# Performance work log

Measured on AMD Instinct MI355X. Metric: run time of the kernel, lower is better.

Reference implementation:

```python
import jax, jax.numpy as jnp
import numpy as np
import math

DIM = 512
HEADS = 8
DIM_HEAD = DIM // HEADS
TIME_DIM = 512
EPS = 1e-5


def _ln(x, g, b):
    m = jnp.mean(x, axis=-1, keepdims=True)
    v = jnp.var(x, axis=-1, keepdims=True)
    return (x - m) * jax.lax.rsqrt(v + EPS) * g + b


def setup_inputs() -> dict:
    key = jax.random.key(0)
    ks = jax.random.split(key, 16)
    s = 0.02
    return {
        "con_features": jax.random.normal(ks[0], (4, 1024, DIM), jnp.float32),
        "diff_features": jax.random.normal(ks[1], (4, 1024, DIM), jnp.float32),
        "time_emb": jax.random.normal(ks[2], (4, TIME_DIM), jnp.float32),
        "ln_con_g": jnp.ones((DIM,), jnp.float32),
        "ln_con_b": jnp.zeros((DIM,), jnp.float32),
        "ln_diff_g": jnp.ones((DIM,), jnp.float32),
        "ln_diff_b": jnp.zeros((DIM,), jnp.float32),
        "wq": jax.random.normal(ks[3], (DIM, DIM), jnp.float32) * s,
        "wk": jax.random.normal(ks[4], (DIM, DIM), jnp.float32) * s,
        "wv": jax.random.normal(ks[5], (DIM, DIM), jnp.float32) * s,
        "w_out": jax.random.normal(ks[6], (DIM, DIM), jnp.float32) * s,
        "b_out": jnp.zeros((DIM,), jnp.float32),
        "w_emd1": jax.random.normal(ks[7], (TIME_DIM, 2 * DIM), jnp.float32) * s,
        "b_emd1": jnp.zeros((2 * DIM,), jnp.float32),
        "w_emd2": jax.random.normal(ks[8], (2 * DIM, 2 * DIM), jnp.float32) * s,
        "b_emd2": jnp.zeros((2 * DIM,), jnp.float32),
        "mlp_ln_g": jnp.ones((DIM,), jnp.float32),
        "mlp_ln_b": jnp.zeros((DIM,), jnp.float32),
        "mlp_w1": jax.random.normal(ks[9], (DIM, DIM), jnp.float32) * s,
        "mlp_b1": jnp.zeros((DIM,), jnp.float32),
        "mlp_w2": jax.random.normal(ks[10], (DIM, DIM), jnp.float32) * s,
        "mlp_b2": jnp.zeros((DIM,), jnp.float32),
    }


def reference(con_features, diff_features, time_emb,
              ln_con_g, ln_con_b, ln_diff_g, ln_diff_b,
              wq, wk, wv, w_out, b_out,
              w_emd1, b_emd1, w_emd2, b_emd2,
              mlp_ln_g, mlp_ln_b, mlp_w1, mlp_b1, mlp_w2, mlp_b2):
    b, n, _ = diff_features.shape
    fea_q = _ln(diff_features, ln_diff_g, ln_diff_b)
    fea_kv = _ln(con_features, ln_con_g, ln_con_b)
    # projections (no bias) + split heads: b n (h d) -> b h n d
    def heads(x):
        return x.reshape(b, n, HEADS, DIM_HEAD).transpose(0, 2, 1, 3)
    q = heads(fea_q @ wq)
    k = heads(fea_kv @ wk)
    v = heads(fea_kv @ wv)
    # 2D FFT over (n, d), ortho norm
    qf = jnp.fft.fft2(q, axes=(-2, -1), norm="ortho")
    kf = jnp.fft.fft2(k, axes=(-2, -1), norm="ortho")
    dots = jnp.einsum("bhnd,bhmd->bhnm", qf, jnp.conj(kf))  # q @ k^H
    attn_c = jnp.fft.ifft2(dots, axes=(-2, -1), norm="ortho")
    mag = jnp.sqrt(attn_c.real ** 2 + attn_c.imag ** 2)
    attn = jax.nn.softmax(mag, axis=-1) / math.sqrt(DIM_HEAD)
    out = jnp.einsum("bhnm,bhmd->bhnd", attn, v)
    out = out.transpose(0, 2, 1, 3).reshape(b, n, DIM)  # b h n d -> b n (h d)
    # global per-sample normalization over (n, dim); torch.std uses ddof=1
    mu = jnp.mean(out, axis=(-2, -1), keepdims=True)
    sd = jnp.std(out, axis=(-2, -1), keepdims=True, ddof=1)
    out1 = (out - mu) / sd
    # FiLM from time embedding
    t = jax.nn.silu(time_emb @ w_emd1 + b_emd1)
    t = t @ w_emd2 + b_emd2
    mean_t, std_t = jnp.split(t, 2, axis=-1)
    out1 = out1 * std_t[:, None, :] + mean_t[:, None, :]
    out1 = out1 @ w_out + b_out
    # FeedForward: LN -> Linear -> GELU(exact) -> Linear
    h = _ln(out1, mlp_ln_g, mlp_ln_b)
    h = jax.nn.gelu(h @ mlp_w1 + mlp_b1, approximate=False)
    return h @ mlp_w2 + mlp_b2
```

## Files before the change

### kernel.cpp

```cpp
#include <hip/hip_runtime.h>
#include <math.h>


typedef _Float16 f16;
typedef _Float16 f16x4 __attribute__((ext_vector_type(4)));
typedef _Float16 f16x8 __attribute__((ext_vector_type(8)));
typedef float f32x4 __attribute__((ext_vector_type(4)));

#define ROWS 4096
#define NTOK 1024
#define NB   4
#define NH   8
#define DH   64

__device__ __forceinline__ void glds16(const f16* g, f16* l) {
    __builtin_amdgcn_global_load_lds((const __attribute__((address_space(1))) void*)g,
                                     (__attribute__((address_space(3))) void*)l, 16, 0, 0);
}

struct PrepArgs { const float* src[6]; f16* dst[6]; };

__device__ __forceinline__ void ln_row(const float* __restrict__ x, const float* __restrict__ g,
                                       const float* __restrict__ bb, f16* __restrict__ o, int lane) {
    float v[8]; float s = 0.f;
#pragma unroll
    for (int j = 0; j < 8; j++) { v[j] = x[lane + 64 * j]; s += v[j]; }
#pragma unroll
    for (int d = 32; d >= 1; d >>= 1) s += __shfl_xor(s, d, 64);
    float mean = s * (1.f / 512.f);
    float q = 0.f;
#pragma unroll
    for (int j = 0; j < 8; j++) { float t = v[j] - mean; q += t * t; }
#pragma unroll
    for (int d = 32; d >= 1; d >>= 1) q += __shfl_xor(q, d, 64);
    float inv = rsqrtf(q * (1.f / 512.f) + 1e-5f);
#pragma unroll
    for (int j = 0; j < 8; j++) {
        int c = lane + 64 * j;
        o[c] = (f16)((v[j] - mean) * inv * g[c] + bb[c]);
    }
}

__global__ __launch_bounds__(256) void k_pre(PrepArgs pa, float* stats,
                                             const float* __restrict__ b_emd1, const float* __restrict__ b_emd2,
                                             float* __restrict__ tbacc, float* __restrict__ filmp,
                                             const float* __restrict__ diff, const float* __restrict__ g_dif,
                                             const float* __restrict__ b_dif, f16* __restrict__ A16,
                                             const float* __restrict__ con, const float* __restrict__ g_con,
                                             const float* __restrict__ b_con, f16* __restrict__ C16) {
    __shared__ float smem[1056];
    const int id = blockIdx.x, tid = threadIdx.x;
    if (id < 16) {
        int o = id * 256 + tid;
        tbacc[o] = b_emd1[o & 1023];
        filmp[o] = b_emd2[o & 1023];
        if (id == 0 && tid < 8) stats[tid] = 0.f;
    } else if (id < 1552) {
        int pid = id - 16;
        int m = pid >> 8, rem = pid & 255;
        int o0 = (rem & 15) * 32, i0 = (rem >> 4) * 32;
        int tx = tid & 31, ty = tid >> 5;
        const float* src = pa.src[m];
        f16* dst = pa.dst[m];
        for (int r = ty; r < 32; r += 8)
            smem[r * 33 + tx] = src[(i0 + r) * 512 + o0 + tx];
        __syncthreads();
        for (int r = ty; r < 32; r += 8)
            dst[(o0 + r) * 512 + i0 + tx] = (f16)smem[tx * 33 + r];
    } else {
        int lane = tid & 63, wid = tid >> 6;
        long row = (long)(id - 1552) * 4 + wid;
        if (row < ROWS) ln_row(diff + row * 512, g_dif, b_dif, A16 + row * 512, lane);
        else { long r = row - ROWS; ln_row(con + r * 512, g_con, b_con, C16 + r * 512, lane); }
    }
}

__global__ __launch_bounds__(256) void k_qkv(const f16* __restrict__ A16, const f16* __restrict__ C16,
                                             const f16* __restrict__ wqT, const f16* __restrict__ wkT,
                                             const f16* __restrict__ wvT,
                                             f16* __restrict__ Qh, f16* __restrict__ Kf, f16* __restrict__ Vt,
                                             const float* __restrict__ temb, const float* __restrict__ w_emd1,
                                             float* __restrict__ tbacc) {
    __shared__ __attribute__((aligned(16))) f16 sh[128 * 128 + 64 * 128];
    const int id = blockIdx.x, tid = threadIdx.x;
    if (id >= 768) {
        float* tsh = (float*)sh;
        int pid = id - 768;
        int c = (pid & 3) * 256 + tid;
        int k0 = (pid >> 2) * 32;
        if (tid < 128) tsh[(tid >> 5) * 32 + (tid & 31)] = temb[(tid >> 5) * 512 + k0 + (tid & 31)];
        __syncthreads();
        float a0 = 0.f, a1 = 0.f, a2 = 0.f, a3 = 0.f;
#pragma unroll 8
        for (int k = 0; k < 32; k++) {
            float w = w_emd1[(k0 + k) * 1024 + c];
            a0 += tsh[k] * w; a1 += tsh[32 + k] * w; a2 += tsh[64 + k] * w; a3 += tsh[96 + k] * w;
        }
        atomicAdd(&tbacc[c], a0);        atomicAdd(&tbacc[1024 + c], a1);
        atomicAdd(&tbacc[2048 + c], a2); atomicAdd(&tbacc[3072 + c], a3);
        return;
    }
    f16* Ash = sh;
    f16* Bsh = sh + 128 * 128;
    const int z = id >> 8;
    const f16* A  = (z == 0) ? A16 : C16;
    const f16* BT = (z == 0) ? wqT : (z == 1) ? wkT : wvT;
    const int lane = tid & 63, wid = tid >> 6;
    const int quad = lane >> 4, l15 = lane & 15;
    const int m0 = (id & 31) * 128, n0 = ((id >> 5) & 7) * 64;
    const int wm = (wid >> 1) * 64, wn = (wid & 1) * 32;
    const int srow = lane >> 4, slot = lane & 15;
    f32x4 acc[4][2] = {};
    for (int kk = 0; kk < 512; kk += 128) {
        if (kk) __syncthreads();
#pragma unroll
        for (int c = 0; c < 8; c++) {
            int r = c * 16 + 4 * wid + srow;
            int j = slot ^ (r & 7);
            glds16(&A[(long)(m0 + r) * 512 + kk + 8 * j], &Ash[(c * 16 + 4 * wid) * 128]);
        }
#pragma unroll
        for (int c = 0; c < 4; c++) {
            int r = c * 16 + 4 * wid + srow;
            int j = slot ^ (r & 7);
            glds16(&BT[(long)(n0 + r) * 512 + kk + 8 * j], &Bsh[(c * 16 + 4 * wid) * 128]);
        }
        __syncthreads();
#pragma unroll
        for (int ks = 0; ks < 4; ks++) {
            const int rslot = ((ks * 4 + quad) ^ (l15 & 7)) * 8;
            f16x8 af[4], bf[2];
#pragma unroll
            for (int t = 0; t < 4; t++)
                af[t] = *(const f16x8*)&Ash[(wm + t * 16 + l15) * 128 + rslot];
#pragma unroll
            for (int t = 0; t < 2; t++)
                bf[t] = *(const f16x8*)&Bsh[(wn + t * 16 + l15) * 128 + rslot];
#pragma unroll
            for (int mt = 0; mt < 4; mt++)
#pragma unroll
                for (int nt = 0; nt < 2; nt++)
                    acc[mt][nt] = __builtin_amdgcn_mfma_f32_16x16x32_f16(af[mt], bf[nt], acc[mt][nt], 0, 0, 0);
        }
    }
    __syncthreads();
    const int bb = m0 >> 10, nn0 = m0 & 1023, h = (id >> 5) & 7;
    if (z <= 1) {
#pragma unroll
        for (int mt = 0; mt < 4; mt++)
#pragma unroll
            for (int nt = 0; nt < 2; nt++)
#pragma unroll
                for (int r = 0; r < 4; r++)
                    sh[(wm + mt * 16 + quad * 4 + r) * 72 + wn + nt * 16 + l15] = (f16)acc[mt][nt][r];
        __syncthreads();
        f16* dst = (z == 0) ? Qh : Kf;
        long basebh = ((long)(bb * NH + h)) * NTOK * DH;
#pragma unroll
        for (int q2 = 0; q2 < 4; q2++) {
            int c = tid + q2 * 256;
            int row = c >> 3, col = (c & 7) * 8;
            int n = nn0 + row;
            int nr = (z == 1) ? ((NTOK - n) & (NTOK - 1)) : n;
            *(f16x8*)&dst[basebh + (long)nr * DH + col] = *(const f16x8*)&sh[row * 72 + col];
        }
    } else {
#pragma unroll
        for (int mt = 0; mt < 4; mt++)
#pragma unroll
            for (int nt = 0; nt < 2; nt++)
#pragma unroll
                for (int r = 0; r < 4; r++)
                    sh[(wn + nt * 16 + l15) * 136 + wm + mt * 16 + quad * 4 + r] = (f16)acc[mt][nt][r];
        __syncthreads();
        long basev = ((long)(bb * NH + h)) * DH * NTOK;
#pragma unroll
        for (int q2 = 0; q2 < 4; q2++) {
            int c = tid + q2 * 256;
            int d = c >> 4, col = (c & 15) * 8;
            *(f16x8*)&Vt[basev + (long)d * NTOK + nn0 + col] = *(const f16x8*)&sh[d * 136 + col];
        }
    }
}

template <int EPI>
__global__ __launch_bounds__(256) void k_gemm64(const f16* __restrict__ A, const f16* __restrict__ BT,
                                                const float* __restrict__ bias, void* __restrict__ dstv) {
    __shared__ __attribute__((aligned(16))) f16 Ash[64 * 128];
    __shared__ __attribute__((aligned(16))) f16 Bsh[64 * 128];
    const int tid = threadIdx.x;
    const int lane = tid & 63, wid = tid >> 6;
    const int quad = lane >> 4, l15 = lane & 15;
    const int m0 = blockIdx.x * 64, n0 = blockIdx.y * 64;
    const int wm = (wid >> 1) * 32, wn = (wid & 1) * 32;
    const int srow = lane >> 4, slot = lane & 15;
    f32x4 acc[2][2] = {};
    for (int kk = 0; kk < 512; kk += 128) {
        if (kk) __syncthreads();
#pragma unroll
        for (int c = 0; c < 4; c++) {
            int r = c * 16 + 4 * wid + srow;
            int j = slot ^ (r & 7);
            glds16(&A[(long)(m0 + r) * 512 + kk + 8 * j], &Ash[(c * 16 + 4 * wid) * 128]);
            glds16(&BT[(long)(n0 + r) * 512 + kk + 8 * j], &Bsh[(c * 16 + 4 * wid) * 128]);
        }
        __syncthreads();
#pragma unroll
        for (int ks = 0; ks < 4; ks++) {
            const int rslot = ((ks * 4 + quad) ^ (l15 & 7)) * 8;
            f16x8 af[2], bf[2];
#pragma unroll
            for (int t = 0; t < 2; t++) {
                af[t] = *(const f16x8*)&Ash[(wm + t * 16 + l15) * 128 + rslot];
                bf[t] = *(const f16x8*)&Bsh[(wn + t * 16 + l15) * 128 + rslot];
            }
#pragma unroll
            for (int mt = 0; mt < 2; mt++)
#pragma unroll
                for (int nt = 0; nt < 2; nt++)
                    acc[mt][nt] = __builtin_amdgcn_mfma_f32_16x16x32_f16(af[mt], bf[nt], acc[mt][nt], 0, 0, 0);
        }
    }
#pragma unroll
    for (int mt = 0; mt < 2; mt++)
#pragma unroll
        for (int nt = 0; nt < 2; nt++)
#pragma unroll
            for (int r = 0; r < 4; r++) {
                int gm = m0 + wm + mt * 16 + quad * 4 + r;
                int gn = n0 + wn + nt * 16 + l15;
                float v = acc[mt][nt][r];
                if (EPI == 3) {
                    float x = v + bias[gn];
                    ((f16*)dstv)[(long)gm * 512 + gn] = (f16)(0.5f * x * (1.0f + erff(x * 0.70710678f)));
                } else {
                    ((float*)dstv)[(long)gm * 512 + gn] = v + bias[gn];
                }
            }
}

__global__ __launch_bounds__(256) void k_gemm2f(const f16* __restrict__ aout16, const float* __restrict__ stats,
                                                const float* __restrict__ filmp,
                                                const f16* __restrict__ BT, const float* __restrict__ bias,
                                                float* __restrict__ out1) {
    __shared__ __attribute__((aligned(16))) f16 Ash[64 * 128];
    __shared__ __attribute__((aligned(16))) f16 Bsh[64 * 128];
    __shared__ float scsh[512], shsh[512];
    const int tid = threadIdx.x;
    const int lane = tid & 63, wid = tid >> 6;
    const int quad = lane >> 4, l15 = lane & 15;
    const int m0 = blockIdx.x * 64, n0 = blockIdx.y * 64;
    const int wm = (wid >> 1) * 32, wn = (wid & 1) * 32;
    const int srow = lane >> 4, slot = lane & 15;
    const int b = m0 >> 10;
    {
        float sum = stats[b * 2], sq = stats[b * 2 + 1];
        const float M = 524288.f;
        float mu = sum / M;
        float isd = rsqrtf((sq - sum * mu) / (M - 1.f));
        for (int c = tid; c < 512; c += 256) {
            float sc = isd * filmp[b * 1024 + 512 + c];
            scsh[c] = sc;
            shsh[c] = filmp[b * 1024 + c] - mu * sc;
        }
    }
    __syncthreads();
    f32x4 acc[2][2] = {};
    for (int kk = 0; kk < 512; kk += 128) {
        if (kk) __syncthreads();
        const int j = slot ^ ((4 * wid + srow) & 7);
        const int gcol = kk + 8 * j;
        float sc[8], sf[8];
        *(float4*)&sc[0] = *(const float4*)&scsh[gcol];
        *(float4*)&sc[4] = *(const float4*)&scsh[gcol + 4];
        *(float4*)&sf[0] = *(const float4*)&shsh[gcol];
        *(float4*)&sf[4] = *(const float4*)&shsh[gcol + 4];
#pragma unroll
        for (int c = 0; c < 4; c++) {
            int r = c * 16 + 4 * wid + srow;
            f16x8 v = *(const f16x8*)&aout16[(long)(m0 + r) * 512 + gcol];
            f16x8 y;
#pragma unroll
            for (int e = 0; e < 8; e++) y[e] = (f16)((float)v[e] * sc[e] + sf[e]);
            *(f16x8*)&Ash[(c * 16 + 4 * wid) * 128 + lane * 8] = y;
            glds16(&BT[(long)(n0 + r) * 512 + kk + 8 * j], &Bsh[(c * 16 + 4 * wid) * 128]);
        }
        __syncthreads();
#pragma unroll
        for (int ks = 0; ks < 4; ks++) {
            const int rslot = ((ks * 4 + quad) ^ (l15 & 7)) * 8;
            f16x8 af[2], bf[2];
#pragma unroll
            for (int t = 0; t < 2; t++) {
                af[t] = *(const f16x8*)&Ash[(wm + t * 16 + l15) * 128 + rslot];
                bf[t] = *(const f16x8*)&Bsh[(wn + t * 16 + l15) * 128 + rslot];
            }
#pragma unroll
            for (int mt = 0; mt < 2; mt++)
#pragma unroll
                for (int nt = 0; nt < 2; nt++)
                    acc[mt][nt] = __builtin_amdgcn_mfma_f32_16x16x32_f16(af[mt], bf[nt], acc[mt][nt], 0, 0, 0);
        }
    }
#pragma unroll
    for (int mt = 0; mt < 2; mt++)
#pragma unroll
        for (int nt = 0; nt < 2; nt++)
#pragma unroll
            for (int r = 0; r < 4; r++) {
                int gm = m0 + wm + mt * 16 + quad * 4 + r;
                int gn = n0 + wn + nt * 16 + l15;
                out1[(long)gm * 512 + gn] = acc[mt][nt][r] + bias[gn];
            }
}

__global__ __launch_bounds__(256) void k_attn(const f16* __restrict__ Q, const f16* __restrict__ Kf,
                                              const f16* __restrict__ Vt, f16* __restrict__ out,
                                              float* __restrict__ stats,
                                              const float* __restrict__ tbacc, const float* __restrict__ w_emd2,
                                              float* __restrict__ filmp) {
    __shared__ __attribute__((aligned(16))) f16 Ksh[128 * 64];
    __shared__ __attribute__((aligned(16))) f16 Vsh[64 * 128];
    __shared__ __attribute__((aligned(16))) f16 PshT[4 * 16 * 136];
    __shared__ float rbuf[8];
    const int id = blockIdx.x, tid = threadIdx.x;
    if (id >= 512) {
        float* tsh = (float*)Ksh;
        int pid = id - 512;
        int c = (pid & 3) * 256 + tid;
        int k0 = (pid >> 2) * 32;
        if (tid < 128) {
            float v = tbacc[(tid >> 5) * 1024 + k0 + (tid & 31)];
            tsh[(tid >> 5) * 32 + (tid & 31)] = v / (1.f + __expf(-v));
        }
        __syncthreads();
        float a0 = 0.f, a1 = 0.f, a2 = 0.f, a3 = 0.f;
#pragma unroll 8
        for (int k = 0; k < 32; k++) {
            float w = w_emd2[(k0 + k) * 1024 + c];
            a0 += tsh[k] * w; a1 += tsh[32 + k] * w; a2 += tsh[64 + k] * w; a3 += tsh[96 + k] * w;
        }
        atomicAdd(&filmp[c], a0);        atomicAdd(&filmp[1024 + c], a1);
        atomicAdd(&filmp[2048 + c], a2); atomicAdd(&filmp[3072 + c], a3);
        return;
    }
    const int lane = tid & 63, wid = tid >> 6;
    const int quad = lane >> 4, l15 = lane & 15;
    const int bh = id & 31;
    const int b = bh >> 3, h = bh & 7, q0 = (id >> 5) * 64;
    const f16* Qbh = Q + (long)bh * NTOK * DH;
    const f16* Kbh = Kf + (long)bh * NTOK * DH;
    const f16* Vbh = Vt + (long)bh * DH * NTOK;
    const int rl = lane >> 3, jj8 = (lane & 7) ^ rl;
    const int rl4 = lane >> 4, jjv = (lane & 15) ^ (4 * wid + rl4);
    const int qrow = q0 + wid * 16 + l15;
    f16x8 qf[2];
    qf[0] = *(const f16x8*)&Qbh[(long)qrow * DH + quad * 8];
    qf[1] = *(const f16x8*)&Qbh[(long)qrow * DH + 32 + quad * 8];
    f32x4 O[4] = {};
    float l_acc = 0.f;
    f16* Pw = PshT + wid * 16 * 136;

    for (int k0 = 0; k0 < NTOK; k0 += 128) {
        if (k0) __syncthreads();
#pragma unroll
        for (int c = 0; c < 4; c++) {
            int rk = c * 32 + 8 * wid + rl;
            glds16(&Kbh[(long)(k0 + rk) * DH + 8 * jj8], &Ksh[(c * 32 + 8 * wid) * 64]);
        }
#pragma unroll
        for (int c = 0; c < 4; c++) {
            int rv = c * 16 + 4 * wid + rl4;
            glds16(&Vbh[(long)rv * NTOK + k0 + 8 * jjv], &Vsh[(c * 16 + 4 * wid) * 128]);
        }
        __syncthreads();
        f32x4 st[8] = {};
#pragma unroll
        for (int ks = 0; ks < 2; ks++) {
            const int slot = ((ks * 4 + quad) ^ (l15 & 7)) * 8;
#pragma unroll
            for (int nt = 0; nt < 8; nt++) {
                f16x8 kf = *(const f16x8*)&Ksh[(nt * 16 + l15) * 64 + slot];
                st[nt] = __builtin_amdgcn_mfma_f32_16x16x32_f16(kf, qf[ks], st[nt], 0, 0, 0);
            }
        }
#pragma unroll
        for (int nt = 0; nt < 8; nt++) {
            float p0 = __expf(fminf(fabsf(st[nt][0]) - 8.f, 11.f));
            float p1 = __expf(fminf(fabsf(st[nt][1]) - 8.f, 11.f));
            float p2 = __expf(fminf(fabsf(st[nt][2]) - 8.f, 11.f));
            float p3 = __expf(fminf(fabsf(st[nt][3]) - 8.f, 11.f));
            l_acc += (p0 + p1) + (p2 + p3);
            f16x4 pk = { (f16)p0, (f16)p1, (f16)p2, (f16)p3 };
            *(f16x4*)&Pw[l15 * 136 + 16 * nt + quad * 4] = pk;
        }
#pragma unroll
        for (int ks = 0; ks < 4; ks++) {
            f16x8 pf = *(const f16x8*)&Pw[l15 * 136 + 32 * ks + quad * 8];
            const int vslot = ((ks * 4 + quad) ^ l15) * 8;
#pragma unroll
            for (int vt = 0; vt < 4; vt++) {
                f16x8 vf = *(const f16x8*)&Vsh[(vt * 16 + l15) * 128 + vslot];
                O[vt] = __builtin_amdgcn_mfma_f32_16x16x32_f16(pf, vf, O[vt], 0, 0, 0);
            }
        }
    }
    l_acc += __shfl_xor(l_acc, 16, 64);
    l_acc += __shfl_xor(l_acc, 32, 64);
    float lb[4];
#pragma unroll
    for (int r = 0; r < 4; r++) lb[r] = 0.125f / __shfl(l_acc, quad * 4 + r, 64);
    float lsum = 0.f, lsq = 0.f;
#pragma unroll
    for (int t = 0; t < 4; t++)
#pragma unroll
        for (int r = 0; r < 4; r++) {
            float v = O[t][r] * lb[r];
            int gn = q0 + wid * 16 + quad * 4 + r;
            int gc = h * DH + t * 16 + l15;
            out[((long)b * NTOK + gn) * 512 + gc] = (f16)v;
            lsum += v; lsq += v * v;
        }
#pragma unroll
    for (int d = 32; d >= 1; d >>= 1) { lsum += __shfl_xor(lsum, d, 64); lsq += __shfl_xor(lsq, d, 64); }
    if (lane == 0) { rbuf[wid] = lsum; rbuf[4 + wid] = lsq; }
    __syncthreads();
    if (tid == 0) {
        atomicAdd(&stats[b * 2], rbuf[0] + rbuf[1] + rbuf[2] + rbuf[3]);
        atomicAdd(&stats[b * 2 + 1], rbuf[4] + rbuf[5] + rbuf[6] + rbuf[7]);
    }
}

__global__ __launch_bounds__(256) void k_ln2(const float* __restrict__ x, const float* __restrict__ g,
                                             const float* __restrict__ bb, f16* __restrict__ o) {
    int lane = threadIdx.x & 63, wid = threadIdx.x >> 6;
    long row = (long)blockIdx.x * 4 + wid;
    ln_row(x + row * 512, g, bb, o + row * 512, lane);
}

extern "C" void kernel_launch(void* const* d_in, const int* in_sizes, int n_in,
                              void* d_out, int out_size, void* d_ws, size_t ws_size,
                              hipStream_t stream) {
    const float* con      = (const float*)d_in[0];
    const float* diff     = (const float*)d_in[1];
    const float* temb     = (const float*)d_in[2];
    const float* ln_con_g = (const float*)d_in[3];
    const float* ln_con_b = (const float*)d_in[4];
    const float* ln_dif_g = (const float*)d_in[5];
    const float* ln_dif_b = (const float*)d_in[6];
    const float* wq       = (const float*)d_in[7];
    const float* wk       = (const float*)d_in[8];
    const float* wv       = (const float*)d_in[9];
    const float* w_out    = (const float*)d_in[10];
    const float* b_out    = (const float*)d_in[11];
    const float* w_emd1   = (const float*)d_in[12];
    const float* b_emd1   = (const float*)d_in[13];
    const float* w_emd2   = (const float*)d_in[14];
    const float* b_emd2   = (const float*)d_in[15];
    const float* mlp_ln_g = (const float*)d_in[16];
    const float* mlp_ln_b = (const float*)d_in[17];
    const float* mlp_w1   = (const float*)d_in[18];
    const float* mlp_b1   = (const float*)d_in[19];
    const float* mlp_w2   = (const float*)d_in[20];
    const float* mlp_b2   = (const float*)d_in[21];
    float* outp = (float*)d_out;

    char* ws = (char*)d_ws;
    size_t off = 0;
    auto alloc = [&](size_t bytes) { void* p = ws + off; off += (bytes + 255) & ~(size_t)255; return p; };
    f16*   A16   = (f16*)alloc((size_t)ROWS * 512 * 2);
    f16*   C16   = (f16*)alloc((size_t)ROWS * 512 * 2);
    f16*   Qh    = (f16*)alloc((size_t)ROWS * 512 * 2);
    f16*   Kf    = (f16*)alloc((size_t)ROWS * 512 * 2);
    f16*   Vt    = (f16*)alloc((size_t)ROWS * 512 * 2);
    f16*   aout16= (f16*)alloc((size_t)ROWS * 512 * 2);
    f16*   wqT   = (f16*)alloc(512 * 512 * 2);
    f16*   wkT   = (f16*)alloc(512 * 512 * 2);
    f16*   wvT   = (f16*)alloc(512 * 512 * 2);
    f16*   woT   = (f16*)alloc(512 * 512 * 2);
    f16*   w1T   = (f16*)alloc(512 * 512 * 2);
    f16*   w2T   = (f16*)alloc(512 * 512 * 2);
    float* tbacc = (float*)alloc(4 * 1024 * 4);
    float* filmp = (float*)alloc(4 * 1024 * 4);
    float* stats = (float*)alloc(256);
    float* out1  = (float*)Qh;
    f16*   X3    = A16;
    f16*   X4    = C16;

    PrepArgs pa;
    pa.src[0] = wq;  pa.src[1] = wk;  pa.src[2] = wv;
    pa.src[3] = w_out; pa.src[4] = mlp_w1; pa.src[5] = mlp_w2;
    pa.dst[0] = wqT; pa.dst[1] = wkT; pa.dst[2] = wvT;
    pa.dst[3] = woT; pa.dst[4] = w1T; pa.dst[5] = w2T;

    k_pre<<<dim3(3600), dim3(256), 0, stream>>>(pa, stats, b_emd1, b_emd2, tbacc, filmp,
                                                diff, ln_dif_g, ln_dif_b, A16,
                                                con, ln_con_g, ln_con_b, C16);
    k_qkv<<<dim3(832), dim3(256), 0, stream>>>(A16, C16, wqT, wkT, wvT, Qh, Kf, Vt,
                                               temb, w_emd1, tbacc);
    k_attn<<<dim3(640), dim3(256), 0, stream>>>(Qh, Kf, Vt, aout16, stats,
                                                tbacc, w_emd2, filmp);
    k_gemm2f<<<dim3(64, 8), dim3(256), 0, stream>>>(aout16, stats, filmp, woT, b_out, out1);
    k_ln2<<<dim3(1024), dim3(256), 0, stream>>>(out1, mlp_ln_g, mlp_ln_b, X3);
    k_gemm64<3><<<dim3(64, 8), dim3(256), 0, stream>>>(X3, w1T, mlp_b1, (void*)X4);
    k_gemm64<4><<<dim3(64, 8), dim3(256), 0, stream>>>(X4, w2T, mlp_b2, (void*)outp);
}
```

Baseline: 184.6 us.

## Fuse MLP LayerNorm into GEMMs via row stats and widen attention query tiles

The out-projection GEMM now writes fp16 output and accumulates per-row sum and sum-of-squares with atomics. The next GEMM applies the LayerNorm while staging A into shared memory, so the separate LN kernel and the fp32 round-trip go away. The attention kernel now handles 32 query rows per wave (128 per block), which halves the block count and reuses each K/V tile across twice as many queries. Risks: computing variance as E[x^2]-mu^2 from fp16-rounded values loses precision, the A-tile load is no longer async, and with fewer attention blocks occupancy drops.

```diff
diff --git a/kernel.cpp b/kernel.cpp
--- a/kernel.cpp
+++ b/kernel.cpp
@@ -44,6 +44,7 @@
 __global__ __launch_bounds__(256) void k_pre(PrepArgs pa, float* stats,
                                              const float* __restrict__ b_emd1, const float* __restrict__ b_emd2,
                                              float* __restrict__ tbacc, float* __restrict__ filmp,
+                                             float* __restrict__ rstats,
                                              const float* __restrict__ diff, const float* __restrict__ g_dif,
                                              const float* __restrict__ b_dif, f16* __restrict__ A16,
                                              const float* __restrict__ con, const float* __restrict__ g_con,
@@ -55,8 +56,10 @@
         tbacc[o] = b_emd1[o & 1023];
         filmp[o] = b_emd2[o & 1023];
         if (id == 0 && tid < 8) stats[tid] = 0.f;
-    } else if (id < 1552) {
-        int pid = id - 16;
+    } else if (id < 48) {
+        rstats[(id - 16) * 256 + tid] = 0.f;
+    } else if (id < 1584) {
+        int pid = id - 48;
         int m = pid >> 8, rem = pid & 255;
         int o0 = (rem & 15) * 32, i0 = (rem >> 4) * 32;
         int tx = tid & 31, ty = tid >> 5;
@@ -69,7 +72,7 @@
             dst[(o0 + r) * 512 + i0 + tx] = (f16)smem[tx * 33 + r];
     } else {
         int lane = tid & 63, wid = tid >> 6;
-        long row = (long)(id - 1552) * 4 + wid;
+        long row = (long)(id - 1584) * 4 + wid;
         if (row < ROWS) ln_row(diff + row * 512, g_dif, b_dif, A16 + row * 512, lane);
         else { long r = row - ROWS; ln_row(con + r * 512, g_con, b_con, C16 + r * 512, lane); }
     }
@@ -183,66 +186,146 @@
     }
 }
 
-template <int EPI>
-__global__ __launch_bounds__(256) void k_gemm64(const f16* __restrict__ A, const f16* __restrict__ BT,
-                                                const float* __restrict__ bias, void* __restrict__ dstv) {
-    __shared__ __attribute__((aligned(16))) f16 Ash[64 * 128];
-    __shared__ __attribute__((aligned(16))) f16 Bsh[64 * 128];
-    const int tid = threadIdx.x;
+__global__ __launch_bounds__(256) void k_attn(const f16* __restrict__ Q, const f16* __restrict__ Kf,
+                                              const f16* __restrict__ Vt, f16* __restrict__ out,
+                                              float* __restrict__ stats,
+                                              const float* __restrict__ tbacc, const float* __restrict__ w_emd2,
+                                              float* __restrict__ filmp) {
+    __shared__ __attribute__((aligned(16))) f16 Ksh[128 * 64];
+    __shared__ __attribute__((aligned(16))) f16 Vsh[64 * 128];
+    __shared__ __attribute__((aligned(16))) f16 PshT[4 * 32 * 136];
+    __shared__ float rbuf[8];
+    const int id = blockIdx.x, tid = threadIdx.x;
+    if (id >= 256) {
+        float* tsh = (float*)Ksh;
+        int pid = id - 256;
+        int c = (pid & 3) * 256 + tid;
+        int k0 = (pid >> 2) * 32;
+        if (tid < 128) {
+            float v = tbacc[(tid >> 5) * 1024 + k0 + (tid & 31)];
+            tsh[(tid >> 5) * 32 + (tid & 31)] = v / (1.f + __expf(-v));
+        }
+        __syncthreads();
+        float a0 = 0.f, a1 = 0.f, a2 = 0.f, a3 = 0.f;
+#pragma unroll 8
+        for (int k = 0; k < 32; k++) {
+            float w = w_emd2[(k0 + k) * 1024 + c];
+            a0 += tsh[k] * w; a1 += tsh[32 + k] * w; a2 += tsh[64 + k] * w; a3 += tsh[96 + k] * w;
+        }
+        atomicAdd(&filmp[c], a0);        atomicAdd(&filmp[1024 + c], a1);
+        atomicAdd(&filmp[2048 + c], a2); atomicAdd(&filmp[3072 + c], a3);
+        return;
+    }
     const int lane = tid & 63, wid = tid >> 6;
     const int quad = lane >> 4, l15 = lane & 15;
-    const int m0 = blockIdx.x * 64, n0 = blockIdx.y * 64;
-    const int wm = (wid >> 1) * 32, wn = (wid & 1) * 32;
-    const int srow = lane >> 4, slot = lane & 15;
-    f32x4 acc[2][2] = {};
-    for (int kk = 0; kk < 512; kk += 128) {
-        if (kk) __syncthreads();
+    const int bh = id & 31;
+    const int b = bh >> 3, hh = bh & 7, q0 = (id >> 5) * 128;
+    const f16* Qbh = Q + (long)bh * NTOK * DH;
+    const f16* Kbh = Kf + (long)bh * NTOK * DH;
+    const f16* Vbh = Vt + (long)bh * DH * NTOK;
+    const int rl = lane >> 3, jj8 = (lane & 7) ^ rl;
+    const int rl4 = lane >> 4, jjv = (lane & 15) ^ (4 * wid + rl4);
+    const int qbase = q0 + wid * 32;
+    f16x8 qf[2][2];
+#pragma unroll
+    for (int h = 0; h < 2; h++) {
+        qf[h][0] = *(const f16x8*)&Qbh[(long)(qbase + 16 * h + l15) * DH + quad * 8];
+        qf[h][1] = *(const f16x8*)&Qbh[(long)(qbase + 16 * h + l15) * DH + 32 + quad * 8];
+    }
+    f32x4 O0[4] = {}, O1[4] = {};
+    float l0 = 0.f, l1 = 0.f;
+    f16* Pw = PshT + wid * 32 * 136;
+
+    for (int k0 = 0; k0 < NTOK; k0 += 128) {
+        if (k0) __syncthreads();
 #pragma unroll
         for (int c = 0; c < 4; c++) {
-            int r = c * 16 + 4 * wid + srow;
-            int j = slot ^ (r & 7);
-            glds16(&A[(long)(m0 + r) * 512 + kk + 8 * j], &Ash[(c * 16 + 4 * wid) * 128]);
-            glds16(&BT[(long)(n0 + r) * 512 + kk + 8 * j], &Bsh[(c * 16 + 4 * wid) * 128]);
-        }
-        __syncthreads();
+            int rk = c * 32 + 8 * wid + rl;
+            glds16(&Kbh[(long)(k0 + rk) * DH + 8 * jj8], &Ksh[(c * 32 + 8 * wid) * 64]);
+        }
+#pragma unroll
+        for (int c = 0; c < 4; c++) {
+            int rv = c * 16 + 4 * wid + rl4;
+            glds16(&Vbh[(long)rv * NTOK + k0 + 8 * jjv], &Vsh[(c * 16 + 4 * wid) * 128]);
+        }
+        __syncthreads();
+        f32x4 st0[8] = {}, st1[8] = {};
+#pragma unroll
+        for (int ks = 0; ks < 2; ks++) {
+            const int slot = ((ks * 4 + quad) ^ (l15 & 7)) * 8;
+#pragma unroll
+            for (int nt = 0; nt < 8; nt++) {
+                f16x8 kf = *(const f16x8*)&Ksh[(nt * 16 + l15) * 64 + slot];
+                st0[nt] = __builtin_amdgcn_mfma_f32_16x16x32_f16(kf, qf[0][ks], st0[nt], 0, 0, 0);
+                st1[nt] = __builtin_amdgcn_mfma_f32_16x16x32_f16(kf, qf[1][ks], st1[nt], 0, 0, 0);
+            }
+        }
+#pragma unroll
+        for (int nt = 0; nt < 8; nt++) {
+            float p0 = __expf(fminf(fabsf(st0[nt][0]) - 8.f, 11.f));
+            float p1 = __expf(fminf(fabsf(st0[nt][1]) - 8.f, 11.f));
+            float p2 = __expf(fminf(fabsf(st0[nt][2]) - 8.f, 11.f));
+            float p3 = __expf(fminf(fabsf(st0[nt][3]) - 8.f, 11.f));
+            l0 += (p0 + p1) + (p2 + p3);
+            f16x4 pk0 = { (f16)p0, (f16)p1, (f16)p2, (f16)p3 };
+            *(f16x4*)&Pw[l15 * 136 + 16 * nt + quad * 4] = pk0;
+            float u0 = __expf(fminf(fabsf(st1[nt][0]) - 8.f, 11.f));
+            float u1 = __expf(fminf(fabsf(st1[nt][1]) - 8.f, 11.f));
+            float u2 = __expf(fminf(fabsf(st1[nt][2]) - 8.f, 11.f));
+            float u3 = __expf(fminf(fabsf(st1[nt][3]) - 8.f, 11.f));
+            l1 += (u0 + u1) + (u2 + u3);
+            f16x4 pk1 = { (f16)u0, (f16)u1, (f16)u2, (f16)u3 };
+            *(f16x4*)&Pw[(16 + l15) * 136 + 16 * nt + quad * 4] = pk1;
+        }
 #pragma unroll
         for (int ks = 0; ks < 4; ks++) {
-            const int rslot = ((ks * 4 + quad) ^ (l15 & 7)) * 8;
-            f16x8 af[2], bf[2];
-#pragma unroll
-            for (int t = 0; t < 2; t++) {
-                af[t] = *(const f16x8*)&Ash[(wm + t * 16 + l15) * 128 + rslot];
-                bf[t] = *(const f16x8*)&Bsh[(wn + t * 16 + l15) * 128 + rslot];
-            }
-#pragma unroll
-            for (int mt = 0; mt < 2; mt++)
-#pragma unroll
-                for (int nt = 0; nt < 2; nt++)
-                    acc[mt][nt] = __builtin_amdgcn_mfma_f32_16x16x32_f16(af[mt], bf[nt], acc[mt][nt], 0, 0, 0);
-        }
-    }
-#pragma unroll
-    for (int mt = 0; mt < 2; mt++)
-#pragma unroll
-        for (int nt = 0; nt < 2; nt++)
-#pragma unroll
-            for (int r = 0; r < 4; r++) {
-                int gm = m0 + wm + mt * 16 + quad * 4 + r;
-                int gn = n0 + wn + nt * 16 + l15;
-                float v = acc[mt][nt][r];
-                if (EPI == 3) {
-                    float x = v + bias[gn];
-                    ((f16*)dstv)[(long)gm * 512 + gn] = (f16)(0.5f * x * (1.0f + erff(x * 0.70710678f)));
-                } else {
-                    ((float*)dstv)[(long)gm * 512 + gn] = v + bias[gn];
-                }
-            }
+            f16x8 pf0 = *(const f16x8*)&Pw[l15 * 136 + 32 * ks + quad * 8];
+            f16x8 pf1 = *(const f16x8*)&Pw[(16 + l15) * 136 + 32 * ks + quad * 8];
+            const int vslot = ((ks * 4 + quad) ^ l15) * 8;
+#pragma unroll
+            for (int vt = 0; vt < 4; vt++) {
+                f16x8 vf = *(const f16x8*)&Vsh[(vt * 16 + l15) * 128 + vslot];
+                O0[vt] = __builtin_amdgcn_mfma_f32_16x16x32_f16(pf0, vf, O0[vt], 0, 0, 0);
+                O1[vt] = __builtin_amdgcn_mfma_f32_16x16x32_f16(pf1, vf, O1[vt], 0, 0, 0);
+            }
+        }
+    }
+    l0 += __shfl_xor(l0, 16, 64); l0 += __shfl_xor(l0, 32, 64);
+    l1 += __shfl_xor(l1, 16, 64); l1 += __shfl_xor(l1, 32, 64);
+    float lb0[4], lb1[4];
+#pragma unroll
+    for (int r = 0; r < 4; r++) {
+        lb0[r] = 0.125f / __shfl(l0, quad * 4 + r, 64);
+        lb1[r] = 0.125f / __shfl(l1, quad * 4 + r, 64);
+    }
+    float lsum = 0.f, lsq = 0.f;
+#pragma unroll
+    for (int t = 0; t < 4; t++)
+#pragma unroll
+        for (int r = 0; r < 4; r++) {
+            float v0 = O0[t][r] * lb0[r];
+            float v1 = O1[t][r] * lb1[r];
+            int gc = hh * DH + t * 16 + l15;
+            int g0 = qbase + quad * 4 + r;
+            int g1 = qbase + 16 + quad * 4 + r;
+            out[((long)b * NTOK + g0) * 512 + gc] = (f16)v0;
+            out[((long)b * NTOK + g1) * 512 + gc] = (f16)v1;
+            lsum += v0 + v1; lsq += v0 * v0 + v1 * v1;
+        }
+#pragma unroll
+    for (int d = 32; d >= 1; d >>= 1) { lsum += __shfl_xor(lsum, d, 64); lsq += __shfl_xor(lsq, d, 64); }
+    if (lane == 0) { rbuf[wid] = lsum; rbuf[4 + wid] = lsq; }
+    __syncthreads();
+    if (tid == 0) {
+        atomicAdd(&stats[b * 2], rbuf[0] + rbuf[1] + rbuf[2] + rbuf[3]);
+        atomicAdd(&stats[b * 2 + 1], rbuf[4] + rbuf[5] + rbuf[6] + rbuf[7]);
+    }
 }
 
 __global__ __launch_bounds__(256) void k_gemm2f(const f16* __restrict__ aout16, const float* __restrict__ stats,
                                                 const float* __restrict__ filmp,
                                                 const f16* __restrict__ BT, const float* __restrict__ bias,
-                                                float* __restrict__ out1) {
+                                                f16* __restrict__ out1h, float* __restrict__ rstats) {
     __shared__ __attribute__((aligned(16))) f16 Ash[64 * 128];
     __shared__ __attribute__((aligned(16))) f16 Bsh[64 * 128];
     __shared__ float scsh[512], shsh[512];
@@ -305,137 +388,145 @@
 #pragma unroll
     for (int mt = 0; mt < 2; mt++)
 #pragma unroll
+        for (int r = 0; r < 4; r++) {
+            int gm = m0 + wm + mt * 16 + quad * 4 + r;
+            float v0 = acc[mt][0][r] + bias[n0 + wn + l15];
+            float v1 = acc[mt][1][r] + bias[n0 + wn + 16 + l15];
+            out1h[(long)gm * 512 + n0 + wn + l15] = (f16)v0;
+            out1h[(long)gm * 512 + n0 + wn + 16 + l15] = (f16)v1;
+            float s = v0 + v1, q2 = v0 * v0 + v1 * v1;
+#pragma unroll
+            for (int d = 8; d >= 1; d >>= 1) { s += __shfl_xor(s, d, 16); q2 += __shfl_xor(q2, d, 16); }
+            if (l15 == 0) {
+                atomicAdd(&rstats[gm * 2], s);
+                atomicAdd(&rstats[gm * 2 + 1], q2);
+            }
+        }
+}
+
+__global__ __launch_bounds__(256) void k_gemm3f(const f16* __restrict__ out1h, const float* __restrict__ rstats,
+                                                const float* __restrict__ lng, const float* __restrict__ lnb,
+                                                const f16* __restrict__ BT, const float* __restrict__ bias,
+                                                f16* __restrict__ X4) {
+    __shared__ __attribute__((aligned(16))) f16 Ash[64 * 128];
+    __shared__ __attribute__((aligned(16))) f16 Bsh[64 * 128];
+    __shared__ float musr[64], invsr[64], gsh[512], bsh[512];
+    const int tid = threadIdx.x;
+    const int lane = tid & 63, wid = tid >> 6;
+    const int quad = lane >> 4, l15 = lane & 15;
+    const int m0 = blockIdx.x * 64, n0 = blockIdx.y * 64;
+    const int wm = (wid >> 1) * 32, wn = (wid & 1) * 32;
+    const int srow = lane >> 4, slot = lane & 15;
+    if (tid < 64) {
+        float s = rstats[(m0 + tid) * 2], sq = rstats[(m0 + tid) * 2 + 1];
+        float mu = s * (1.f / 512.f);
+        float var = sq * (1.f / 512.f) - mu * mu;
+        musr[tid] = mu;
+        invsr[tid] = rsqrtf(var + 1e-5f);
+    }
+    for (int i = tid; i < 512; i += 256) { gsh[i] = lng[i]; bsh[i] = lnb[i]; }
+    __syncthreads();
+    f32x4 acc[2][2] = {};
+    for (int kk = 0; kk < 512; kk += 128) {
+        if (kk) __syncthreads();
+        const int j = slot ^ ((4 * wid + srow) & 7);
+        const int gcol = kk + 8 * j;
+        float gv[8], bv[8];
+        *(float4*)&gv[0] = *(const float4*)&gsh[gcol];
+        *(float4*)&gv[4] = *(const float4*)&gsh[gcol + 4];
+        *(float4*)&bv[0] = *(const float4*)&bsh[gcol];
+        *(float4*)&bv[4] = *(const float4*)&bsh[gcol + 4];
+#pragma unroll
+        for (int c = 0; c < 4; c++) {
+            int r = c * 16 + 4 * wid + srow;
+            f16x8 x = *(const f16x8*)&out1h[(long)(m0 + r) * 512 + gcol];
+            float a = invsr[r], m = musr[r];
+            f16x8 y;
+#pragma unroll
+            for (int e = 0; e < 8; e++) {
+                float sc = a * gv[e];
+                y[e] = (f16)((float)x[e] * sc + (bv[e] - m * sc));
+            }
+            *(f16x8*)&Ash[(c * 16 + 4 * wid) * 128 + lane * 8] = y;
+            glds16(&BT[(long)(n0 + r) * 512 + kk + 8 * j], &Bsh[(c * 16 + 4 * wid) * 128]);
+        }
+        __syncthreads();
+#pragma unroll
+        for (int ks = 0; ks < 4; ks++) {
+            const int rslot = ((ks * 4 + quad) ^ (l15 & 7)) * 8;
+            f16x8 af[2], bf[2];
+#pragma unroll
+            for (int t = 0; t < 2; t++) {
+                af[t] = *(const f16x8*)&Ash[(wm + t * 16 + l15) * 128 + rslot];
+                bf[t] = *(const f16x8*)&Bsh[(wn + t * 16 + l15) * 128 + rslot];
+            }
+#pragma unroll
+            for (int mt = 0; mt < 2; mt++)
+#pragma unroll
+                for (int nt = 0; nt < 2; nt++)
+                    acc[mt][nt] = __builtin_amdgcn_mfma_f32_16x16x32_f16(af[mt], bf[nt], acc[mt][nt], 0, 0, 0);
+        }
+    }
+#pragma unroll
+    for (int mt = 0; mt < 2; mt++)
+#pragma unroll
         for (int nt = 0; nt < 2; nt++)
 #pragma unroll
             for (int r = 0; r < 4; r++) {
                 int gm = m0 + wm + mt * 16 + quad * 4 + r;
                 int gn = n0 + wn + nt * 16 + l15;
-                out1[(long)gm * 512 + gn] = acc[mt][nt][r] + bias[gn];
-            }
-}
-
-__global__ __launch_bounds__(256) void k_attn(const f16* __restrict__ Q, const f16* __restrict__ Kf,
-                                              const f16* __restrict__ Vt, f16* __restrict__ out,
-                                              float* __restrict__ stats,
-                                              const float* __restrict__ tbacc, const float* __restrict__ w_emd2,
-                                              float* __restrict__ filmp) {
-    __shared__ __attribute__((aligned(16))) f16 Ksh[128 * 64];
-    __shared__ __attribute__((aligned(16))) f16 Vsh[64 * 128];
-    __shared__ __attribute__((aligned(16))) f16 PshT[4 * 16 * 136];
-    __shared__ float rbuf[8];
-    const int id = blockIdx.x, tid = threadIdx.x;
-    if (id >= 512) {
-        float* tsh = (float*)Ksh;
-        int pid = id - 512;
-        int c = (pid & 3) * 256 + tid;
-        int k0 = (pid >> 2) * 32;
-        if (tid < 128) {
-            float v = tbacc[(tid >> 5) * 1024 + k0 + (tid & 31)];
-            tsh[(tid >> 5) * 32 + (tid & 31)] = v / (1.f + __expf(-v));
-        }
-        __syncthreads();
-        float a0 = 0.f, a1 = 0.f, a2 = 0.f, a3 = 0.f;
-#pragma unroll 8
-        for (int k = 0; k < 32; k++) {
-            float w = w_emd2[(k0 + k) * 1024 + c];
-            a0 += tsh[k] * w; a1 += tsh[32 + k] * w; a2 += tsh[64 + k] * w; a3 += tsh[96 + k] * w;
-        }
-        atomicAdd(&filmp[c], a0);        atomicAdd(&filmp[1024 + c], a1);
-        atomicAdd(&filmp[2048 + c], a2); atomicAdd(&filmp[3072 + c], a3);
-        return;
-    }
+                float x = acc[mt][nt][r] + bias[gn];
+                X4[(long)gm * 512 + gn] = (f16)(0.5f * x * (1.0f + erff(x * 0.70710678f)));
+            }
+}
+
+__global__ __launch_bounds__(256) void k_gemm4(const f16* __restrict__ A, const f16* __restrict__ BT,
+                                               const float* __restrict__ bias, float* __restrict__ dst) {
+    __shared__ __attribute__((aligned(16))) f16 Ash[64 * 128];
+    __shared__ __attribute__((aligned(16))) f16 Bsh[64 * 128];
+    const int tid = threadIdx.x;
     const int lane = tid & 63, wid = tid >> 6;
     const int quad = lane >> 4, l15 = lane & 15;
-    const int bh = id & 31;
-    const int b = bh >> 3, h = bh & 7, q0 = (id >> 5) * 64;
-    const f16* Qbh = Q + (long)bh * NTOK * DH;
-    const f16* Kbh = Kf + (long)bh * NTOK * DH;
-    const f16* Vbh = Vt + (long)bh * DH * NTOK;
-    const int rl = lane >> 3, jj8 = (lane & 7) ^ rl;
-    const int rl4 = lane >> 4, jjv = (lane & 15) ^ (4 * wid + rl4);
-    const int qrow = q0 + wid * 16 + l15;
-    f16x8 qf[2];
-    qf[0] = *(const f16x8*)&Qbh[(long)qrow * DH + quad * 8];
-    qf[1] = *(const f16x8*)&Qbh[(long)qrow * DH + 32 + quad * 8];
-    f32x4 O[4] = {};
-    float l_acc = 0.f;
-    f16* Pw = PshT + wid * 16 * 136;
-
-    for (int k0 = 0; k0 < NTOK; k0 += 128) {
-        if (k0) __syncthreads();
+    const int m0 = blockIdx.x * 64, n0 = blockIdx.y * 64;
+    const int wm = (wid >> 1) * 32, wn = (wid & 1) * 32;
+    const int srow = lane >> 4, slot = lane & 15;
+    f32x4 acc[2][2] = {};
+    for (int kk = 0; kk < 512; kk += 128) {
+        if (kk) __syncthreads();
 #pragma unroll
         for (int c = 0; c < 4; c++) {
-            int rk = c * 32 + 8 * wid + rl;
-            glds16(&Kbh[(long)(k0 + rk) * DH + 8 * jj8], &Ksh[(c * 32 + 8 * wid) * 64]);
-        }
-#pragma unroll
-        for (int c = 0; c < 4; c++) {
-            int rv = c * 16 + 4 * wid + rl4;
-            glds16(&Vbh[(long)rv * NTOK + k0 + 8 * jjv], &Vsh[(c * 16 + 4 * wid) * 128]);
-        }
-        __syncthreads();
-        f32x4 st[8] = {};
-#pragma unroll
-        for (int ks = 0; ks < 2; ks++) {
-            const int slot = ((ks * 4 + quad) ^ (l15 & 7)) * 8;
-#pragma unroll
-            for (int nt = 0; nt < 8; nt++) {
-                f16x8 kf = *(const f16x8*)&Ksh[(nt * 16 + l15) * 64 + slot];
-                st[nt] = __builtin_amdgcn_mfma_f32_16x16x32_f16(kf, qf[ks], st[nt], 0, 0, 0);
-            }
-        }
-#pragma unroll
-        for (int nt = 0; nt < 8; nt++) {
-            float p0 = __expf(fminf(fabsf(st[nt][0]) - 8.f, 11.f));
-            float p1 = __expf(fminf(fabsf(st[nt][1]) - 8.f, 11.f));
-            float p2 = __expf(fminf(fabsf(st[nt][2]) - 8.f, 11.f));
-            float p3 = __expf(fminf(fabsf(st[nt][3]) - 8.f, 11.f));
-            l_acc += (p0 + p1) + (p2 + p3);
-            f16x4 pk = { (f16)p0, (f16)p1, (f16)p2, (f16)p3 };
-            *(f16x4*)&Pw[l15 * 136 + 16 * nt + quad * 4] = pk;
-        }
+            int r = c * 16 + 4 * wid + srow;
+            int j = slot ^ (r & 7);
+            glds16(&A[(long)(m0 + r) * 512 + kk + 8 * j], &Ash[(c * 16 + 4 * wid) * 128]);
+            glds16(&BT[(long)(n0 + r) * 512 + kk + 8 * j], &Bsh[(c * 16 + 4 * wid) * 128]);
+        }
+        __syncthreads();
 #pragma unroll
         for (int ks = 0; ks < 4; ks++) {
-            f16x8 pf = *(const f16x8*)&Pw[l15 * 136 + 32 * ks + quad * 8];
-            const int vslot = ((ks * 4 + quad) ^ l15) * 8;
-#pragma unroll
-            for (int vt = 0; vt < 4; vt++) {
-                f16x8 vf = *(const f16x8*)&Vsh[(vt * 16 + l15) * 128 + vslot];
-                O[vt] = __builtin_amdgcn_mfma_f32_16x16x32_f16(pf, vf, O[vt], 0, 0, 0);
-            }
-        }
-    }
-    l_acc += __shfl_xor(l_acc, 16, 64);
-    l_acc += __shfl_xor(l_acc, 32, 64);
-    float lb[4];
-#pragma unroll
-    for (int r = 0; r < 4; r++) lb[r] = 0.125f / __shfl(l_acc, quad * 4 + r, 64);
-    float lsum = 0.f, lsq = 0.f;
-#pragma unroll
-    for (int t = 0; t < 4; t++)
-#pragma unroll
-        for (int r = 0; r < 4; r++) {
-            float v = O[t][r] * lb[r];
-            int gn = q0 + wid * 16 + quad * 4 + r;
-            int gc = h * DH + t * 16 + l15;
-            out[((long)b * NTOK + gn) * 512 + gc] = (f16)v;
-            lsum += v; lsq += v * v;
-        }
-#pragma unroll
-    for (int d = 32; d >= 1; d >>= 1) { lsum += __shfl_xor(lsum, d, 64); lsq += __shfl_xor(lsq, d, 64); }
-    if (lane == 0) { rbuf[wid] = lsum; rbuf[4 + wid] = lsq; }
-    __syncthreads();
-    if (tid == 0) {
-        atomicAdd(&stats[b * 2], rbuf[0] + rbuf[1] + rbuf[2] + rbuf[3]);
-        atomicAdd(&stats[b * 2 + 1], rbuf[4] + rbuf[5] + rbuf[6] + rbuf[7]);
-    }
-}
-
-__global__ __launch_bounds__(256) void k_ln2(const float* __restrict__ x, const float* __restrict__ g,
-                                             const float* __restrict__ bb, f16* __restrict__ o) {
-    int lane = threadIdx.x & 63, wid = threadIdx.x >> 6;
-    long row = (long)blockIdx.x * 4 + wid;
-    ln_row(x + row * 512, g, bb, o + row * 512, lane);
+            const int rslot = ((ks * 4 + quad) ^ (l15 & 7)) * 8;
+            f16x8 af[2], bf[2];
+#pragma unroll
+            for (int t = 0; t < 2; t++) {
+                af[t] = *(const f16x8*)&Ash[(wm + t * 16 + l15) * 128 + rslot];
+                bf[t] = *(const f16x8*)&Bsh[(wn + t * 16 + l15) * 128 + rslot];
+            }
+#pragma unroll
+            for (int mt = 0; mt < 2; mt++)
+#pragma unroll
+                for (int nt = 0; nt < 2; nt++)
+                    acc[mt][nt] = __builtin_amdgcn_mfma_f32_16x16x32_f16(af[mt], bf[nt], acc[mt][nt], 0, 0, 0);
+        }
+    }
+#pragma unroll
+    for (int mt = 0; mt < 2; mt++)
+#pragma unroll
+        for (int nt = 0; nt < 2; nt++)
+#pragma unroll
+            for (int r = 0; r < 4; r++) {
+                int gm = m0 + wm + mt * 16 + quad * 4 + r;
+                int gn = n0 + wn + nt * 16 + l15;
+                dst[(long)gm * 512 + gn] = acc[mt][nt][r] + bias[gn];
+            }
 }
 
 extern "C" void kernel_launch(void* const* d_in, const int* in_sizes, int n_in,
@@ -483,8 +574,8 @@
     float* tbacc = (float*)alloc(4 * 1024 * 4);
     float* filmp = (float*)alloc(4 * 1024 * 4);
     float* stats = (float*)alloc(256);
-    float* out1  = (float*)Qh;
-    f16*   X3    = A16;
+    float* rstats= (float*)alloc(ROWS * 2 * 4);
+    f16*   out1h = Qh;
     f16*   X4    = C16;
 
     PrepArgs pa;
@@ -493,15 +584,14 @@
     pa.dst[0] = wqT; pa.dst[1] = wkT; pa.dst[2] = wvT;
     pa.dst[3] = woT; pa.dst[4] = w1T; pa.dst[5] = w2T;
 
-    k_pre<<<dim3(3600), dim3(256), 0, stream>>>(pa, stats, b_emd1, b_emd2, tbacc, filmp,
+    k_pre<<<dim3(3632), dim3(256), 0, stream>>>(pa, stats, b_emd1, b_emd2, tbacc, filmp, rstats,
                                                 diff, ln_dif_g, ln_dif_b, A16,
                                                 con, ln_con_g, ln_con_b, C16);
     k_qkv<<<dim3(832), dim3(256), 0, stream>>>(A16, C16, wqT, wkT, wvT, Qh, Kf, Vt,
                                                temb, w_emd1, tbacc);
-    k_attn<<<dim3(640), dim3(256), 0, stream>>>(Qh, Kf, Vt, aout16, stats,
+    k_attn<<<dim3(384), dim3(256), 0, stream>>>(Qh, Kf, Vt, aout16, stats,
                                                 tbacc, w_emd2, filmp);
-    k_gemm2f<<<dim3(64, 8), dim3(256), 0, stream>>>(aout16, stats, filmp, woT, b_out, out1);
-    k_ln2<<<dim3(1024), dim3(256), 0, stream>>>(out1, mlp_ln_g, mlp_ln_b, X3);
-    k_gemm64<3><<<dim3(64, 8), dim3(256), 0, stream>>>(X3, w1T, mlp_b1, (void*)X4);
-    k_gemm64<4><<<dim3(64, 8), dim3(256), 0, stream>>>(X4, w2T, mlp_b2, (void*)outp);
-}
+    k_gemm2f<<<dim3(64, 8), dim3(256), 0, stream>>>(aout16, stats, filmp, woT, b_out, out1h, rstats);
+    k_gemm3f<<<dim3(64, 8), dim3(256), 0, stream>>>(out1h, rstats, mlp_ln_g, mlp_ln_b, w1T, mlp_b1, X4);
+    k_gemm4<<<dim3(64, 8), dim3(256), 0, stream>>>(X4, w2T, mlp_b2, outp);
+}
```

Result: no change. 186.8 us (+1.2%).
